# Kernel optimization log

Hardware: AMD Instinct MI355X
Metric: run time of the kernel (lower is better)

## Reference

```python
import jax, jax.numpy as jnp
import numpy as np

N_NODES = 200000
N_EDGES = 3200000
VOCAB = 10000
D = 25
EPS = 1e-5


def setup_inputs() -> dict:
    key = jax.random.key(0)
    ks = jax.random.split(key, 16)
    x = jax.random.randint(ks[0], (N_NODES,), 0, VOCAB)
    edge_index = jax.random.randint(ks[1], (2, N_EDGES), 0, N_NODES)
    s = 1.0 / np.sqrt(D)
    inp = {
        'x': x,
        'edge_index': edge_index,
        'emb': jax.random.normal(ks[2], (VOCAB, D), jnp.float32),
        'W1': jax.random.normal(ks[3], (D, D), jnp.float32) * s,
        'b1': jnp.zeros((D,), jnp.float32),
        'g1': jnp.ones((D,), jnp.float32),
        'be1': jnp.zeros((D,), jnp.float32),
        'W2': jax.random.normal(ks[4], (D, D), jnp.float32) * s,
        'b2': jnp.zeros((D,), jnp.float32),
        'g2': jnp.ones((D,), jnp.float32),
        'be2': jnp.zeros((D,), jnp.float32),
        'Wm1': jax.random.normal(ks[5], (D, 12), jnp.float32) * s,
        'bm1': jnp.zeros((12,), jnp.float32),
        'Wm2': jax.random.normal(ks[6], (12, 1), jnp.float32) * (1.0 / np.sqrt(12)),
        'bm2': jnp.zeros((1,), jnp.float32),
    }
    return inp


def gcn_conv(h, src, dst, W, b):
    # PyG GCNConv: h @ W, symmetric normalization with self-loops, scatter-add, + bias
    n = h.shape[0]
    h = h @ W
    loops = jnp.arange(n)
    s = jnp.concatenate([src, loops])  # sources j
    d = jnp.concatenate([dst, loops])  # targets i
    deg = jax.ops.segment_sum(jnp.ones_like(d, h.dtype), d, num_segments=n)
    dinv = jnp.where(deg > 0, jax.lax.rsqrt(jnp.maximum(deg, 1.0)), 0.0)
    norm = dinv[s] * dinv[d]  # [E+N]
    msg = h[s] * norm[:, None]
    out = jax.ops.segment_sum(msg, d, num_segments=n)
    return out + b


def batch_norm(h, g, b):
    mu = jnp.mean(h, axis=0)
    var = jnp.mean((h - mu) ** 2, axis=0)
    return (h - mu) * jax.lax.rsqrt(var + EPS) * g + b


def reference(x, edge_index, emb, W1, b1, g1, be1, W2, b2, g2, be2, Wm1, bm1, Wm2, bm2):
    src, dst = edge_index[0], edge_index[1]
    h = emb[x]  # [N, 25]
    h = jax.nn.relu(batch_norm(gcn_conv(h, src, dst, W1, b1), g1, be1))
    h = jax.nn.relu(batch_norm(gcn_conv(h, src, dst, W2, b2), g2, be2))
    h = jax.nn.relu(h @ Wm1 + bm1)
    return jax.nn.sigmoid(h @ Wm2 + bm2)  # [N, 1]
```

## Files before the change

### kernel.cpp

```cpp
#include <hip/hip_runtime.h>
#include <hip/hip_fp16.h>
#include <math.h>

#define D 25
#define PH_STRIDE 32
#define STATS_BLOCKS 512
#define NBK 256
#define BIN_EDGES 8192
#define NSLOT 64
#define EPS 1e-5f

__global__ __launch_bounds__(256) void binA(const int* __restrict__ dst,
                                            int* __restrict__ hist2D,
                                            float* __restrict__ stPart, int E) {
    if (blockIdx.x < 25) stPart[blockIdx.x * 256 + threadIdx.x] = 0.0f;
    __shared__ int h[NBK];
    h[threadIdx.x] = 0;
    __syncthreads();
    int base = blockIdx.x * BIN_EDGES;
#pragma unroll
    for (int j = 0; j < 32; ++j) {
        int idx = base + j * 256 + threadIdx.x;
        if (idx < E) atomicAdd(&h[dst[idx] >> 10], 1);
    }
    __syncthreads();
    hist2D[blockIdx.x * NBK + threadIdx.x] = h[threadIdx.x];
}

__global__ __launch_bounds__(512) void colscan(int* __restrict__ hist2D,
                                               int* __restrict__ bCount, int nbBin) {
    __shared__ int s[512];
    int b = blockIdx.x;
    int j = threadIdx.x;
    int v = (j < nbBin) ? hist2D[j * NBK + b] : 0;
    s[j] = v;
    __syncthreads();
    for (int off = 1; off < 512; off <<= 1) {
        int x = (j >= off) ? s[j - off] : 0;
        __syncthreads();
        s[j] += x;
        __syncthreads();
    }
    if (j < nbBin) hist2D[j * NBK + b] = s[j] - v;
    if (j == 0) bCount[b] = s[511];
}

__global__ __launch_bounds__(256) void binB(const int* __restrict__ src,
                                            const int* __restrict__ dst,
                                            const int* __restrict__ hist2D,
                                            const int* __restrict__ bCount,
                                            int* __restrict__ binned, int E) {
    __shared__ int rank[NBK], basew[NBK], sc[NBK];
    int t = threadIdx.x;
    int cnt = bCount[t];
    sc[t] = cnt;
    rank[t] = 0;
    __syncthreads();
    for (int off = 1; off < NBK; off <<= 1) {
        int x = (t >= off) ? sc[t - off] : 0;
        __syncthreads();
        sc[t] += x;
        __syncthreads();
    }
    basew[t] = (sc[t] - cnt) + hist2D[blockIdx.x * NBK + t];
    __syncthreads();
    int base = blockIdx.x * BIN_EDGES;
#pragma unroll
    for (int j = 0; j < 32; ++j) {
        int idx = base + j * 256 + t;
        if (idx < E) {
            int d = dst[idx];
            int b = d >> 10;
            int r = atomicAdd(&rank[b], 1);
            binned[basew[b] + r] = (src[idx] << 10) | (d & 1023);
        }
    }
}

__global__ __launch_bounds__(512) void fill_embed(
        const int* __restrict__ binned, const int* __restrict__ bCount,
        const int* __restrict__ x, const float* __restrict__ emb,
        const float* __restrict__ W1,
        int* __restrict__ degi, int* __restrict__ cursor, int* __restrict__ csr,
        __half* __restrict__ Ph, int N) {
    int b = blockIdx.x;
    int nodeBase = b << 10;
    if (nodeBase >= N) return;
    __shared__ int h[1024];
    __shared__ int s2[512];
    __shared__ float sW[D * D];
    int t = threadIdx.x;
    if (t < 256) s2[t] = (t < b) ? bCount[t] : 0;
    for (int j = t; j < D * D; j += 512) sW[j] = W1[j];
    __syncthreads();
    for (int off = 128; off > 0; off >>= 1) {
        if (t < 128 && t < off) s2[t] += s2[t + off];
        __syncthreads();
    }
    int s = s2[0];
    __syncthreads();
    h[t] = 0; h[t + 512] = 0;
    __syncthreads();
    int e = s + bCount[b];
    for (int k = s + t; k < e; k += 512)
        atomicAdd(&h[binned[k] & 1023], 1);
    __syncthreads();
    int i0 = t * 2;
    int v0 = h[i0], v1 = h[i0 + 1];
    int node0 = nodeBase + i0;
    if (node0 < N) degi[node0] = v0;
    if (node0 + 1 < N) degi[node0 + 1] = v1;
    s2[t] = v0 + v1;
    __syncthreads();
    for (int off = 1; off < 512; off <<= 1) {
        int xx = (t >= off) ? s2[t - off] : 0;
        __syncthreads();
        s2[t] += xx;
        __syncthreads();
    }
    int pre = (t > 0) ? s2[t - 1] : 0;
    h[i0] = pre;
    h[i0 + 1] = pre + v0;
    __syncthreads();
    for (int k = s + t; k < e; k += 512) {
        int key = binned[k];
        int p = atomicAdd(&h[key & 1023], 1);
        csr[s + p] = key >> 10;
    }
    __syncthreads();
    if (node0 < N) cursor[node0] = s + h[i0];
    if (node0 + 1 < N) cursor[node0 + 1] = s + h[i0 + 1];
#pragma unroll
    for (int which = 0; which < 2; ++which) {
        int node = node0 + which;
        if (node >= N) break;
        int dg = which ? v1 : v0;
        const float* er = emb + (size_t)x[node] * D;
        float tv[D];
#pragma unroll
        for (int k = 0; k < D; ++k) tv[k] = er[k];
        float dinv = rsqrtf((float)dg + 1.0f);
        __half* row = Ph + (size_t)node * PH_STRIDE;
#pragma unroll
        for (int d = 0; d < D; ++d) {
            float acc = 0.0f;
#pragma unroll
            for (int k = 0; k < D; ++k) acc = fmaf(tv[k], sW[k * D + d], acc);
            row[d] = __float2half(dinv * acc);
        }
#pragma unroll
        for (int d = D; d < PH_STRIDE; ++d) row[d] = __float2half(0.0f);
    }
}

__global__ __launch_bounds__(256) void gather_stats_w8(
        const int* __restrict__ csr, const int* __restrict__ cursor,
        const int* __restrict__ degi, const __half* __restrict__ Ph,
        const float* __restrict__ bias, __half* __restrict__ Qh,
        float* __restrict__ stPart, int N) {
    int t = threadIdx.x;
    int node = blockIdx.x * 16 + (t >> 4);
    int f = t & 15;
    const __half2* rowb = (const __half2*)Ph;
    float q0 = 0.0f, q1 = 0.0f;
    if (node < N) {
        int end = cursor[node];
        int dg = degi[node];
        int k = end - dg;
        float2 sv = __half22float2(rowb[((size_t)node << 4) + f]);
        float ax = sv.x, ay = sv.y;
        for (; k + 8 <= end; k += 8) {
            int s0 = csr[k],     s1 = csr[k + 1], s2 = csr[k + 2], s3 = csr[k + 3];
            int s4 = csr[k + 4], s5 = csr[k + 5], s6 = csr[k + 6], s7 = csr[k + 7];
            float2 v0 = __half22float2(rowb[((size_t)s0 << 4) + f]);
            float2 v1 = __half22float2(rowb[((size_t)s1 << 4) + f]);
            float2 v2 = __half22float2(rowb[((size_t)s2 << 4) + f]);
            float2 v3 = __half22float2(rowb[((size_t)s3 << 4) + f]);
            float2 v4 = __half22float2(rowb[((size_t)s4 << 4) + f]);
            float2 v5 = __half22float2(rowb[((size_t)s5 << 4) + f]);
            float2 v6 = __half22float2(rowb[((size_t)s6 << 4) + f]);
            float2 v7 = __half22float2(rowb[((size_t)s7 << 4) + f]);
            ax += ((v0.x + v1.x) + (v2.x + v3.x)) + ((v4.x + v5.x) + (v6.x + v7.x));
            ay += ((v0.y + v1.y) + (v2.y + v3.y)) + ((v4.y + v5.y) + (v6.y + v7.y));
        }
        for (; k + 4 <= end; k += 4) {
            int s0 = csr[k], s1 = csr[k + 1], s2 = csr[k + 2], s3 = csr[k + 3];
            float2 v0 = __half22float2(rowb[((size_t)s0 << 4) + f]);
            float2 v1 = __half22float2(rowb[((size_t)s1 << 4) + f]);
            float2 v2 = __half22float2(rowb[((size_t)s2 << 4) + f]);
            float2 v3 = __half22float2(rowb[((size_t)s3 << 4) + f]);
            ax += (v0.x + v1.x) + (v2.x + v3.x);
            ay += (v0.y + v1.y) + (v2.y + v3.y);
        }
        for (; k < end; ++k) {
            float2 v = __half22float2(rowb[((size_t)csr[k] << 4) + f]);
            ax += v.x; ay += v.y;
        }
        float dinv = rsqrtf((float)dg + 1.0f);
        if (f < 13) {
            int j0 = f << 1;
            q0 = fmaf(dinv, ax, bias[j0]);
            if (f < 12) q1 = fmaf(dinv, ay, bias[j0 + 1]);
            ((__half2*)Qh)[((size_t)node << 4) + f] = __floats2half2_rn(q0, q1);
        }
    }
    float ls0 = q0, lq0 = q0 * q0, ls1 = q1, lq1 = q1 * q1;
    ls0 += __shfl_down(ls0, 32, 64); ls0 += __shfl_down(ls0, 16, 64);
    lq0 += __shfl_down(lq0, 32, 64); lq0 += __shfl_down(lq0, 16, 64);
    ls1 += __shfl_down(ls1, 32, 64); ls1 += __shfl_down(ls1, 16, 64);
    lq1 += __shfl_down(lq1, 32, 64); lq1 += __shfl_down(lq1, 16, 64);
    __shared__ float red[4][16][4];
    if ((t & 63) < 16) {
        int w = t >> 6;
        red[w][f][0] = ls0; red[w][f][1] = lq0;
        red[w][f][2] = ls1; red[w][f][3] = lq1;
    }
    __syncthreads();
    if (t < 64) {
        int ff = t >> 2, slot = t & 3;
        float tot = red[0][ff][slot] + red[1][ff][slot] + red[2][ff][slot] + red[3][ff][slot];
        int a = 2 * ff + (slot >> 1);
        if (a < D) atomicAdd(&stPart[(blockIdx.x & (NSLOT - 1)) * 50 + a + (slot & 1) * D], tot);
    }
}

__global__ __launch_bounds__(256) void bn_gemm_hp(
        const __half* __restrict__ Qh, const float* __restrict__ stPart, float invN,
        const float* __restrict__ g, const float* __restrict__ be,
        const float* __restrict__ W, const int* __restrict__ degi,
        __half* __restrict__ Ph, int N) {
    __shared__ float sW[D * D];
    __shared__ float sScale[D], sShift[D];
    __shared__ float sSum[2 * D];
    for (int j = threadIdx.x; j < D * D; j += blockDim.x) sW[j] = W[j];
    if (threadIdx.x < 2 * D) {
        float a = 0.0f;
        for (int k = 0; k < NSLOT; ++k) a += stPart[k * 50 + threadIdx.x];
        sSum[threadIdx.x] = a;
    }
    __syncthreads();
    if (threadIdx.x < D) {
        float m = sSum[threadIdx.x] * invN;
        float v = fmaxf(sSum[D + threadIdx.x] * invN - m * m, 0.0f);
        float sc = rsqrtf(v + EPS) * g[threadIdx.x];
        sScale[threadIdx.x] = sc;
        sShift[threadIdx.x] = be[threadIdx.x] - m * sc;
    }
    __syncthreads();
    int i = blockIdx.x * blockDim.x + threadIdx.x;
    if (i >= N) return;
    const __half2* qrow = (const __half2*)Qh + ((size_t)i << 4);
    float t[D];
#pragma unroll
    for (int ff = 0; ff < 13; ++ff) {
        float2 v = __half22float2(qrow[ff]);
        int j0 = ff << 1;
        t[j0] = fmaxf(0.0f, fmaf(v.x, sScale[j0], sShift[j0]));
        if (ff < 12) t[j0 + 1] = fmaxf(0.0f, fmaf(v.y, sScale[j0 + 1], sShift[j0 + 1]));
    }
    float dinv = rsqrtf((float)degi[i] + 1.0f);
    __half* row = Ph + (size_t)i * PH_STRIDE;
#pragma unroll
    for (int d = 0; d < D; ++d) {
        float acc = 0.0f;
#pragma unroll
        for (int k = 0; k < D; ++k) acc = fmaf(t[k], sW[k * D + d], acc);
        row[d] = __float2half(dinv * acc);
    }
#pragma unroll
    for (int d = D; d < PH_STRIDE; ++d) row[d] = __float2half(0.0f);
}

__global__ __launch_bounds__(256) void final_kernel_p(
        const __half* __restrict__ Qh, const float* __restrict__ stPart, float invN,
        const float* __restrict__ g, const float* __restrict__ be,
        const float* __restrict__ Wm1, const float* __restrict__ bm1,
        const float* __restrict__ Wm2, const float* __restrict__ bm2,
        float* __restrict__ out, int N) {
    __shared__ float sW1[D * 12];
    __shared__ float sb1[12], sW2[12];
    __shared__ float sScale[D], sShift[D];
    __shared__ float sSum[2 * D];
    __shared__ float sb2;
    for (int j = threadIdx.x; j < D * 12; j += blockDim.x) sW1[j] = Wm1[j];
    if (threadIdx.x < 12) {
        sb1[threadIdx.x] = bm1[threadIdx.x];
        sW2[threadIdx.x] = Wm2[threadIdx.x];
    }
    if (threadIdx.x < 2 * D) {
        float a = 0.0f;
        for (int k = 0; k < NSLOT; ++k) a += stPart[k * 50 + threadIdx.x];
        sSum[threadIdx.x] = a;
    }
    if (threadIdx.x == 0) sb2 = bm2[0];
    __syncthreads();
    if (threadIdx.x < D) {
        float m = sSum[threadIdx.x] * invN;
        float v = fmaxf(sSum[D + threadIdx.x] * invN - m * m, 0.0f);
        float sc = rsqrtf(v + EPS) * g[threadIdx.x];
        sScale[threadIdx.x] = sc;
        sShift[threadIdx.x] = be[threadIdx.x] - m * sc;
    }
    __syncthreads();
    int i = blockIdx.x * blockDim.x + threadIdx.x;
    if (i >= N) return;
    const __half2* qrow = (const __half2*)Qh + ((size_t)i << 4);
    float t[D];
#pragma unroll
    for (int ff = 0; ff < 13; ++ff) {
        float2 v = __half22float2(qrow[ff]);
        int j0 = ff << 1;
        t[j0] = fmaxf(0.0f, fmaf(v.x, sScale[j0], sShift[j0]));
        if (ff < 12) t[j0 + 1] = fmaxf(0.0f, fmaf(v.y, sScale[j0 + 1], sShift[j0 + 1]));
    }
    float z = sb2;
#pragma unroll
    for (int j = 0; j < 12; ++j) {
        float m = sb1[j];
#pragma unroll
        for (int k = 0; k < D; ++k) m = fmaf(t[k], sW1[k * 12 + j], m);
        m = fmaxf(0.0f, m);
        z = fmaf(m, sW2[j], z);
    }
    out[i] = 1.0f / (1.0f + expf(-z));
}

__global__ void hist_kernel(const int* __restrict__ dst, int* __restrict__ degi, int E) {
    int e = blockIdx.x * blockDim.x + threadIdx.x;
    if (e < E) atomicAdd(&degi[dst[e]], 1);
}

__global__ __launch_bounds__(256) void embed_gemm1(
        const int* __restrict__ x, const float* __restrict__ emb,
        const float* __restrict__ W1, const int* __restrict__ degi,
        float* __restrict__ P, float* __restrict__ Qdup, int N) {
    __shared__ float sW[D * D];
    for (int j = threadIdx.x; j < D * D; j += blockDim.x) sW[j] = W1[j];
    __syncthreads();
    int i = blockIdx.x * blockDim.x + threadIdx.x;
    if (i >= N) return;
    const float* er = emb + (size_t)x[i] * D;
    float t[D];
#pragma unroll
    for (int k = 0; k < D; ++k) t[k] = er[k];
    float dinv = rsqrtf((float)degi[i] + 1.0f);
#pragma unroll
    for (int d = 0; d < D; ++d) {
        float acc = 0.0f;
#pragma unroll
        for (int k = 0; k < D; ++k) acc = fmaf(t[k], sW[k * D + d], acc);
        float v = dinv * acc;
        P[i * D + d] = v;
        if (Qdup) Qdup[i * D + d] = v;
    }
}

__global__ void scatter_kernel(const int* __restrict__ src, const int* __restrict__ dst,
                               const float* __restrict__ A, float* __restrict__ B, int E) {
    int idx = blockIdx.x * blockDim.x + threadIdx.x;
    int e = idx >> 5;
    int lane = idx & 31;
    if (e >= E || lane >= D) return;
    atomicAdd(&B[dst[e] * D + lane], A[src[e] * D + lane]);
}

__global__ __launch_bounds__(256) void transform_kernel(
        float* __restrict__ Q, const int* __restrict__ degi,
        const float* __restrict__ bias, int N) {
    int i = blockIdx.x * blockDim.x + threadIdx.x;
    if (i >= N) return;
    float dinv = rsqrtf((float)degi[i] + 1.0f);
#pragma unroll
    for (int d = 0; d < D; ++d)
        Q[i * D + d] = fmaf(dinv, Q[i * D + d], bias[d]);
}

__global__ __launch_bounds__(256) void stats_kernel(
        const float* __restrict__ Q, float* __restrict__ st, int N) {
    float ls[D], lq[D];
#pragma unroll
    for (int d = 0; d < D; ++d) { ls[d] = 0.0f; lq[d] = 0.0f; }
    for (int i = blockIdx.x * blockDim.x + threadIdx.x; i < N;
         i += gridDim.x * blockDim.x) {
#pragma unroll
        for (int d = 0; d < D; ++d) {
            float v = Q[i * D + d];
            ls[d] += v;
            lq[d] += v * v;
        }
    }
#pragma unroll
    for (int d = 0; d < D; ++d) {
        for (int off = 32; off > 0; off >>= 1) {
            ls[d] += __shfl_down(ls[d], off, 64);
            lq[d] += __shfl_down(lq[d], off, 64);
        }
    }
    __shared__ float red[4][2 * D];
    int wave = threadIdx.x >> 6;
    int lane = threadIdx.x & 63;
    if (lane == 0) {
#pragma unroll
        for (int d = 0; d < D; ++d) {
            red[wave][d] = ls[d];
            red[wave][D + d] = lq[d];
        }
    }
    __syncthreads();
    if (threadIdx.x < 2 * D) {
        float t = red[0][threadIdx.x] + red[1][threadIdx.x] +
                  red[2][threadIdx.x] + red[3][threadIdx.x];
        atomicAdd(&st[threadIdx.x], t);
    }
}

__global__ __launch_bounds__(256) void bn_gemm(
        const float* __restrict__ Qin, const float* __restrict__ st, float invN,
        const float* __restrict__ g, const float* __restrict__ be,
        const float* __restrict__ W, const int* __restrict__ degi,
        float* __restrict__ P, float* __restrict__ Qdup, int N) {
    __shared__ float sW[D * D];
    __shared__ float sScale[D], sShift[D];
    for (int j = threadIdx.x; j < D * D; j += blockDim.x) sW[j] = W[j];
    if (threadIdx.x < D) {
        float m = st[threadIdx.x] * invN;
        float v = fmaxf(st[D + threadIdx.x] * invN - m * m, 0.0f);
        float sc = rsqrtf(v + EPS) * g[threadIdx.x];
        sScale[threadIdx.x] = sc;
        sShift[threadIdx.x] = be[threadIdx.x] - m * sc;
    }
    __syncthreads();
    int i = blockIdx.x * blockDim.x + threadIdx.x;
    if (i >= N) return;
    float t[D];
#pragma unroll
    for (int d = 0; d < D; ++d)
        t[d] = fmaxf(0.0f, fmaf(Qin[i * D + d], sScale[d], sShift[d]));
    float dinv = rsqrtf((float)degi[i] + 1.0f);
#pragma unroll
    for (int d = 0; d < D; ++d) {
        float acc = 0.0f;
#pragma unroll
        for (int k = 0; k < D; ++k) acc = fmaf(t[k], sW[k * D + d], acc);
        float v = dinv * acc;
        P[i * D + d] = v;
        if (Qdup) Qdup[i * D + d] = v;
    }
}

__global__ __launch_bounds__(256) void final_kernel(
        const float* __restrict__ Q, const float* __restrict__ st, float invN,
        const float* __restrict__ g, const float* __restrict__ be,
        const float* __restrict__ Wm1, const float* __restrict__ bm1,
        const float* __restrict__ Wm2, const float* __restrict__ bm2,
        float* __restrict__ out, int N) {
    __shared__ float sW1[D * 12];
    __shared__ float sb1[12], sW2[12];
    __shared__ float sScale[D], sShift[D];
    __shared__ float sb2;
    for (int j = threadIdx.x; j < D * 12; j += blockDim.x) sW1[j] = Wm1[j];
    if (threadIdx.x < 12) {
        sb1[threadIdx.x] = bm1[threadIdx.x];
        sW2[threadIdx.x] = Wm2[threadIdx.x];
    }
    if (threadIdx.x < D) {
        float m = st[threadIdx.x] * invN;
        float v = fmaxf(st[D + threadIdx.x] * invN - m * m, 0.0f);
        float sc = rsqrtf(v + EPS) * g[threadIdx.x];
        sScale[threadIdx.x] = sc;
        sShift[threadIdx.x] = be[threadIdx.x] - m * sc;
    }
    if (threadIdx.x == 0) sb2 = bm2[0];
    __syncthreads();
    int i = blockIdx.x * blockDim.x + threadIdx.x;
    if (i >= N) return;
    float t[D];
#pragma unroll
    for (int d = 0; d < D; ++d)
        t[d] = fmaxf(0.0f, fmaf(Q[i * D + d], sScale[d], sShift[d]));
    float z = sb2;
#pragma unroll
    for (int j = 0; j < 12; ++j) {
        float m = sb1[j];
#pragma unroll
        for (int k = 0; k < D; ++k) m = fmaf(t[k], sW1[k * 12 + j], m);
        m = fmaxf(0.0f, m);
        z = fmaf(m, sW2[j], z);
    }
    out[i] = 1.0f / (1.0f + expf(-z));
}

extern "C" void kernel_launch(void* const* d_in, const int* in_sizes, int n_in,
                              void* d_out, int out_size, void* d_ws, size_t ws_size,
                              hipStream_t stream) {
    const int*   x    = (const int*)d_in[0];
    const int*   ei   = (const int*)d_in[1];
    const float* emb  = (const float*)d_in[2];
    const float* W1   = (const float*)d_in[3];
    const float* b1   = (const float*)d_in[4];
    const float* g1   = (const float*)d_in[5];
    const float* be1  = (const float*)d_in[6];
    const float* W2   = (const float*)d_in[7];
    const float* b2   = (const float*)d_in[8];
    const float* g2   = (const float*)d_in[9];
    const float* be2  = (const float*)d_in[10];
    const float* Wm1  = (const float*)d_in[11];
    const float* bm1  = (const float*)d_in[12];
    const float* Wm2  = (const float*)d_in[13];
    const float* bm2  = (const float*)d_in[14];
    float* out = (float*)d_out;

    int N = in_sizes[0];
    int E = in_sizes[1] / 2;
    const int* src = ei;
    const int* dst = ei + E;
    float invN = 1.0f / (float)N;

    int nbBin = (E + BIN_EDGES - 1) / BIN_EDGES;
    size_t csrNeed = ((size_t)34 * N + E + 256 + (size_t)nbBin * NBK + 2 * NSLOT * 50) * 4;
    bool useCSR = (ws_size >= csrNeed) && (N <= NBK * 1024) && (nbBin <= 512) &&
                  ((size_t)E <= (size_t)16 * N) && (nbBin >= 25);

    int nbN  = (N + 255) / 256;
    int nbE  = (E + 255) / 256;
    int nbG  = (N + 15) / 16;
    int nbS  = (int)(((long)E * 32 + 255) / 256);

    if (useCSR) {
        int*    degi    = (int*)d_ws;
        int*    cursor  = degi + N;
        int*    csr     = cursor + N;
        int*    bCount  = csr + E;
        int*    hist2D  = bCount + NBK;
        __half* Ph      = (__half*)(hist2D + (size_t)nbBin * NBK);
        __half* Qh      = Ph + (size_t)N * PH_STRIDE;
        float*  stP1    = (float*)(Qh + (size_t)N * PH_STRIDE);
        float*  stP2    = stP1 + NSLOT * 50;
        int*    binned  = (int*)Qh;

        int nbBkt = (N + 1023) / 1024;

        binA<<<nbBin, 256, 0, stream>>>(dst, hist2D, stP1, E);
        colscan<<<NBK, 512, 0, stream>>>(hist2D, bCount, nbBin);
        binB<<<nbBin, 256, 0, stream>>>(src, dst, hist2D, bCount, binned, E);
        fill_embed<<<nbBkt, 512, 0, stream>>>(binned, bCount, x, emb, W1,
                                              degi, cursor, csr, Ph, N);
        gather_stats_w8<<<nbG, 256, 0, stream>>>(csr, cursor, degi, Ph, b1, Qh, stP1, N);
        bn_gemm_hp<<<nbN, 256, 0, stream>>>(Qh, stP1, invN, g1, be1, W2, degi, Ph, N);
        gather_stats_w8<<<nbG, 256, 0, stream>>>(csr, cursor, degi, Ph, b2, Qh, stP2, N);
        final_kernel_p<<<nbN, 256, 0, stream>>>(Qh, stP2, invN, g2, be2, Wm1, bm1, Wm2, bm2, out, N);
    } else {
        int*   degi  = (int*)d_ws;
        float* P     = (float*)(degi + N);
        float* Q     = P + (size_t)N * D;
        float* stats = Q + (size_t)N * D;
        float* st1 = stats;
        float* st2 = stats + 50;

        hipMemsetAsync(degi, 0, (size_t)N * sizeof(int), stream);
        hipMemsetAsync(stats, 0, 100 * sizeof(float), stream);

        hist_kernel<<<nbE, 256, 0, stream>>>(dst, degi, E);
        embed_gemm1<<<nbN, 256, 0, stream>>>(x, emb, W1, degi, P, Q, N);
        scatter_kernel<<<nbS, 256, 0, stream>>>(src, dst, P, Q, E);
        transform_kernel<<<nbN, 256, 0, stream>>>(Q, degi, b1, N);
        stats_kernel<<<STATS_BLOCKS, 256, 0, stream>>>(Q, st1, N);
        bn_gemm<<<nbN, 256, 0, stream>>>(Q, st1, invN, g1, be1, W2, degi, P, Q, N);
        scatter_kernel<<<nbS, 256, 0, stream>>>(src, dst, P, Q, E);
        transform_kernel<<<nbN, 256, 0, stream>>>(Q, degi, b2, N);
        stats_kernel<<<STATS_BLOCKS, 256, 0, stream>>>(Q, st2, N);
        final_kernel<<<nbN, 256, 0, stream>>>(Q, st2, invN, g2, be2, Wm1, bm1, Wm2, bm2, out, N);
    }
}
```

Before: 332.4 us.

## Use finer 512-node buckets, LDS-staged CSR fill, split embedding GEMM into own kernel

Bucket width drops from 1024 to 512 nodes, so the CSR build launches about twice as many blocks, and binB now runs with 512 threads. The bucket fill sorts each bucket's source indices in shared memory and then writes the CSR slice contiguously, replacing scattered global writes. The embedding times W1 step moves out of the fill kernel into a separate one-thread-per-node kernel, which adds a launch but frees the fill kernel from the GEMM's register and occupancy pressure. Extra LDS for the sort buffer may limit blocks per CU.

```diff
diff --git a/kernel.cpp b/kernel.cpp
--- a/kernel.cpp
+++ b/kernel.cpp
@@ -5,8 +5,11 @@
 #define D 25
 #define PH_STRIDE 32
 #define STATS_BLOCKS 512
-#define NBK 256
+#define NBKT 512
+#define BSH 9
+#define BMSK 511
 #define BIN_EDGES 8192
+#define SORT_CAP 10240
 #define NSLOT 64
 #define EPS 1e-5f
 
@@ -14,17 +17,19 @@
                                             int* __restrict__ hist2D,
                                             float* __restrict__ stPart, int E) {
     if (blockIdx.x < 25) stPart[blockIdx.x * 256 + threadIdx.x] = 0.0f;
-    __shared__ int h[NBK];
+    __shared__ int h[NBKT];
     h[threadIdx.x] = 0;
+    h[threadIdx.x + 256] = 0;
     __syncthreads();
     int base = blockIdx.x * BIN_EDGES;
 #pragma unroll
     for (int j = 0; j < 32; ++j) {
         int idx = base + j * 256 + threadIdx.x;
-        if (idx < E) atomicAdd(&h[dst[idx] >> 10], 1);
-    }
-    __syncthreads();
-    hist2D[blockIdx.x * NBK + threadIdx.x] = h[threadIdx.x];
+        if (idx < E) atomicAdd(&h[dst[idx] >> BSH], 1);
+    }
+    __syncthreads();
+    hist2D[blockIdx.x * NBKT + threadIdx.x] = h[threadIdx.x];
+    hist2D[blockIdx.x * NBKT + threadIdx.x + 256] = h[threadIdx.x + 256];
 }
 
 __global__ __launch_bounds__(512) void colscan(int* __restrict__ hist2D,
@@ -32,7 +37,7 @@
     __shared__ int s[512];
     int b = blockIdx.x;
     int j = threadIdx.x;
-    int v = (j < nbBin) ? hist2D[j * NBK + b] : 0;
+    int v = (j < nbBin) ? hist2D[j * NBKT + b] : 0;
     s[j] = v;
     __syncthreads();
     for (int off = 1; off < 512; off <<= 1) {
@@ -41,116 +46,124 @@
         s[j] += x;
         __syncthreads();
     }
-    if (j < nbBin) hist2D[j * NBK + b] = s[j] - v;
+    if (j < nbBin) hist2D[j * NBKT + b] = s[j] - v;
     if (j == 0) bCount[b] = s[511];
 }
 
-__global__ __launch_bounds__(256) void binB(const int* __restrict__ src,
+__global__ __launch_bounds__(512) void binB(const int* __restrict__ src,
                                             const int* __restrict__ dst,
                                             const int* __restrict__ hist2D,
                                             const int* __restrict__ bCount,
                                             int* __restrict__ binned, int E) {
-    __shared__ int rank[NBK], basew[NBK], sc[NBK];
+    __shared__ int rank[NBKT], basew[NBKT], sc[NBKT];
     int t = threadIdx.x;
     int cnt = bCount[t];
     sc[t] = cnt;
     rank[t] = 0;
     __syncthreads();
-    for (int off = 1; off < NBK; off <<= 1) {
+    for (int off = 1; off < NBKT; off <<= 1) {
         int x = (t >= off) ? sc[t - off] : 0;
         __syncthreads();
         sc[t] += x;
         __syncthreads();
     }
-    basew[t] = (sc[t] - cnt) + hist2D[blockIdx.x * NBK + t];
+    basew[t] = (sc[t] - cnt) + hist2D[blockIdx.x * NBKT + t];
     __syncthreads();
     int base = blockIdx.x * BIN_EDGES;
 #pragma unroll
-    for (int j = 0; j < 32; ++j) {
-        int idx = base + j * 256 + t;
+    for (int j = 0; j < 16; ++j) {
+        int idx = base + j * 512 + t;
         if (idx < E) {
             int d = dst[idx];
-            int b = d >> 10;
+            int b = d >> BSH;
             int r = atomicAdd(&rank[b], 1);
-            binned[basew[b] + r] = (src[idx] << 10) | (d & 1023);
-        }
-    }
-}
-
-__global__ __launch_bounds__(512) void fill_embed(
+            binned[basew[b] + r] = (src[idx] << BSH) | (d & BMSK);
+        }
+    }
+}
+
+__global__ __launch_bounds__(512) void bucket_fill(
         const int* __restrict__ binned, const int* __restrict__ bCount,
+        int* __restrict__ degi, int* __restrict__ cursor, int* __restrict__ csr, int N) {
+    int b = blockIdx.x;
+    int nodeBase = b << BSH;
+    if (nodeBase >= N) return;
+    __shared__ int h[NBKT];
+    __shared__ int s2[512];
+    __shared__ int sorted[SORT_CAP];
+    int t = threadIdx.x;
+    s2[t] = (t < b) ? bCount[t] : 0;
+    __syncthreads();
+    for (int off = 256; off > 0; off >>= 1) {
+        if (t < off) s2[t] += s2[t + off];
+        __syncthreads();
+    }
+    int s = s2[0];
+    __syncthreads();
+    h[t] = 0;
+    __syncthreads();
+    int cnt = bCount[b];
+    int e = s + cnt;
+    for (int k = s + t; k < e; k += 512)
+        atomicAdd(&h[binned[k] & BMSK], 1);
+    __syncthreads();
+    int dg = h[t];
+    int node = nodeBase + t;
+    if (node < N) degi[node] = dg;
+    s2[t] = dg;
+    __syncthreads();
+    for (int off = 1; off < 512; off <<= 1) {
+        int x = (t >= off) ? s2[t - off] : 0;
+        __syncthreads();
+        s2[t] += x;
+        __syncthreads();
+    }
+    int start = s2[t] - dg;
+    h[t] = start;
+    if (node < N) cursor[node] = s + s2[t];
+    __syncthreads();
+    if (cnt <= SORT_CAP) {
+        for (int k = s + t; k < e; k += 512) {
+            int key = binned[k];
+            int p = atomicAdd(&h[key & BMSK], 1);
+            sorted[p] = key >> BSH;
+        }
+        __syncthreads();
+        for (int j = t; j < cnt; j += 512)
+            csr[s + j] = sorted[j];
+    } else {
+        for (int k = s + t; k < e; k += 512) {
+            int key = binned[k];
+            int p = atomicAdd(&h[key & BMSK], 1);
+            csr[s + p] = key >> BSH;
+        }
+    }
+}
+
+__global__ __launch_bounds__(256) void embed_gemm1_h(
         const int* __restrict__ x, const float* __restrict__ emb,
-        const float* __restrict__ W1,
-        int* __restrict__ degi, int* __restrict__ cursor, int* __restrict__ csr,
+        const float* __restrict__ W1, const int* __restrict__ degi,
         __half* __restrict__ Ph, int N) {
-    int b = blockIdx.x;
-    int nodeBase = b << 10;
-    if (nodeBase >= N) return;
-    __shared__ int h[1024];
-    __shared__ int s2[512];
     __shared__ float sW[D * D];
-    int t = threadIdx.x;
-    if (t < 256) s2[t] = (t < b) ? bCount[t] : 0;
-    for (int j = t; j < D * D; j += 512) sW[j] = W1[j];
-    __syncthreads();
-    for (int off = 128; off > 0; off >>= 1) {
-        if (t < 128 && t < off) s2[t] += s2[t + off];
-        __syncthreads();
-    }
-    int s = s2[0];
-    __syncthreads();
-    h[t] = 0; h[t + 512] = 0;
-    __syncthreads();
-    int e = s + bCount[b];
-    for (int k = s + t; k < e; k += 512)
-        atomicAdd(&h[binned[k] & 1023], 1);
-    __syncthreads();
-    int i0 = t * 2;
-    int v0 = h[i0], v1 = h[i0 + 1];
-    int node0 = nodeBase + i0;
-    if (node0 < N) degi[node0] = v0;
-    if (node0 + 1 < N) degi[node0 + 1] = v1;
-    s2[t] = v0 + v1;
-    __syncthreads();
-    for (int off = 1; off < 512; off <<= 1) {
-        int xx = (t >= off) ? s2[t - off] : 0;
-        __syncthreads();
-        s2[t] += xx;
-        __syncthreads();
-    }
-    int pre = (t > 0) ? s2[t - 1] : 0;
-    h[i0] = pre;
-    h[i0 + 1] = pre + v0;
-    __syncthreads();
-    for (int k = s + t; k < e; k += 512) {
-        int key = binned[k];
-        int p = atomicAdd(&h[key & 1023], 1);
-        csr[s + p] = key >> 10;
-    }
-    __syncthreads();
-    if (node0 < N) cursor[node0] = s + h[i0];
-    if (node0 + 1 < N) cursor[node0 + 1] = s + h[i0 + 1];
-#pragma unroll
-    for (int which = 0; which < 2; ++which) {
-        int node = node0 + which;
-        if (node >= N) break;
-        int dg = which ? v1 : v0;
-        const float* er = emb + (size_t)x[node] * D;
-        float tv[D];
-#pragma unroll
-        for (int k = 0; k < D; ++k) tv[k] = er[k];
-        float dinv = rsqrtf((float)dg + 1.0f);
-        __half* row = Ph + (size_t)node * PH_STRIDE;
-#pragma unroll
-        for (int d = 0; d < D; ++d) {
-            float acc = 0.0f;
-#pragma unroll
-            for (int k = 0; k < D; ++k) acc = fmaf(tv[k], sW[k * D + d], acc);
-            row[d] = __float2half(dinv * acc);
-        }
-#pragma unroll
-        for (int d = D; d < PH_STRIDE; ++d) row[d] = __float2half(0.0f);
-    }
+    for (int j = threadIdx.x; j < D * D; j += blockDim.x) sW[j] = W1[j];
+    __syncthreads();
+    int i = blockIdx.x * blockDim.x + threadIdx.x;
+    if (i >= N) return;
+    const float* er = emb + (size_t)x[i] * D;
+    float t[D];
+#pragma unroll
+    for (int k = 0; k < D; ++k) t[k] = er[k];
+    float dinv = rsqrtf((float)degi[i] + 1.0f);
+    __half* row = Ph + (size_t)i * PH_STRIDE;
+#pragma unroll
+    for (int d = 0; d < D; ++d) {
+        float acc = 0.0f;
+#pragma unroll
+        for (int k = 0; k < D; ++k) acc = fmaf(t[k], sW[k * D + d], acc);
+        row[d] = __float2half(dinv * acc);
+    }
+#pragma unroll
+    for (int d = D; d < PH_STRIDE; ++d) row[d] = __float2half(0.0f);
 }
 
 __global__ __launch_bounds__(256) void gather_stats_w8(
@@ -517,8 +530,8 @@
     float invN = 1.0f / (float)N;
 
     int nbBin = (E + BIN_EDGES - 1) / BIN_EDGES;
-    size_t csrNeed = ((size_t)34 * N + E + 256 + (size_t)nbBin * NBK + 2 * NSLOT * 50) * 4;
-    bool useCSR = (ws_size >= csrNeed) && (N <= NBK * 1024) && (nbBin <= 512) &&
+    size_t csrNeed = ((size_t)34 * N + E + 512 + (size_t)nbBin * NBKT + 2 * NSLOT * 50) * 4;
+    bool useCSR = (ws_size >= csrNeed) && (N <= NBKT * 512) && (nbBin <= 512) &&
                   ((size_t)E <= (size_t)16 * N) && (nbBin >= 25);
 
     int nbN  = (N + 255) / 256;
@@ -531,20 +544,20 @@
         int*    cursor  = degi + N;
         int*    csr     = cursor + N;
         int*    bCount  = csr + E;
-        int*    hist2D  = bCount + NBK;
-        __half* Ph      = (__half*)(hist2D + (size_t)nbBin * NBK);
+        int*    hist2D  = bCount + NBKT;
+        __half* Ph      = (__half*)(hist2D + (size_t)nbBin * NBKT);
         __half* Qh      = Ph + (size_t)N * PH_STRIDE;
         float*  stP1    = (float*)(Qh + (size_t)N * PH_STRIDE);
         float*  stP2    = stP1 + NSLOT * 50;
         int*    binned  = (int*)Qh;
 
-        int nbBkt = (N + 1023) / 1024;
+        int nbBkt = (N + 511) / 512;
 
         binA<<<nbBin, 256, 0, stream>>>(dst, hist2D, stP1, E);
-        colscan<<<NBK, 512, 0, stream>>>(hist2D, bCount, nbBin);
-        binB<<<nbBin, 256, 0, stream>>>(src, dst, hist2D, bCount, binned, E);
-        fill_embed<<<nbBkt, 512, 0, stream>>>(binned, bCount, x, emb, W1,
-                                              degi, cursor, csr, Ph, N);
+        colscan<<<NBKT, 512, 0, stream>>>(hist2D, bCount, nbBin);
+        binB<<<nbBin, 512, 0, stream>>>(src, dst, hist2D, bCount, binned, E);
+        bucket_fill<<<nbBkt, 512, 0, stream>>>(binned, bCount, degi, cursor, csr, N);
+        embed_gemm1_h<<<nbN, 256, 0, stream>>>(x, emb, W1, degi, Ph, N);
         gather_stats_w8<<<nbG, 256, 0, stream>>>(csr, cursor, degi, Ph, b1, Qh, stP1, N);
         bn_gemm_hp<<<nbN, 256, 0, stream>>>(Qh, stP1, invN, g1, be1, W2, degi, Ph, N);
         gather_stats_w8<<<nbG, 256, 0, stream>>>(csr, cursor, degi, Ph, b2, Qh, stP2, N);
```

New measurement: 308.8 us, median of 2. 7.1% less time.
